# Kernel tuning notes

Measured on AMD Instinct MI355X. Metric: run time of the kernel, lower is better.

The kernel has to match this reference:

```python
import jax, jax.numpy as jnp
import numpy as np

N, E = 100_000, 1_600_000
NDIM_IN, EDIM, F, H, C = 64, 32, 32, 3, 10  # F=ndim_out per head, H=num_heads


def _edge_softmax(scores, dst, n):
    # softmax over incoming edges grouped by destination node (DGL edge_softmax)
    m = jax.ops.segment_max(scores, dst, num_segments=n)          # [N,H]
    ex = jnp.exp(scores - m[dst])                                  # [E,H]
    s = jax.ops.segment_sum(ex, dst, num_segments=n)               # [N,H]
    return ex / s[dst]


def _egat_conv(nf, ef, src, dst, W, We, al, ar, ae, b, n):
    # DGL EdgeGATConv: edge features modulate attention logits only
    h, f = al.shape
    ft = (nf @ W).reshape(-1, h, f)      # [N,H,F]
    fe = (ef @ We).reshape(-1, h, f)     # [E,H,F]
    el = (ft * al).sum(-1)               # [N,H]
    er = (ft * ar).sum(-1)               # [N,H]
    ee = (fe * ae).sum(-1)               # [E,H]
    e = jax.nn.leaky_relu(el[src] + er[dst] + ee, 0.2)             # [E,H]
    a = _edge_softmax(e, dst, n)                                   # [E,H]
    rst = jax.ops.segment_sum(ft[src] * a[:, :, None], dst, num_segments=n)
    return rst + b.reshape(1, h, f)


def setup_inputs() -> dict:
    key = jax.random.key(0)
    ks = jax.random.split(key, 16)
    s = lambda k, shp, fan: (jax.random.normal(k, shp, jnp.float32) / np.sqrt(fan).astype(np.float32))
    d = {}
    d["nfeats"] = jax.random.normal(ks[0], (N, 1, NDIM_IN), jnp.float32)
    d["efeats"] = jax.random.normal(ks[1], (E, 1, EDIM), jnp.float32)
    d["src"] = jax.random.randint(ks[2], (E,), 0, N, jnp.int32)
    d["dst"] = jax.random.randint(ks[3], (E,), 0, N, jnp.int32)
    # conv1 params
    d["W1"] = s(ks[4], (NDIM_IN, H * F), NDIM_IN)
    d["We1"] = s(ks[5], (EDIM, H * F), EDIM)
    d["al1"] = s(ks[6], (H, F), F)
    d["ar1"] = s(ks[7], (H, F), F)
    d["ae1"] = s(ks[8], (H, F), F)
    d["b1"] = jnp.zeros((H * F,), jnp.float32)
    # conv2 params (input dim = H*F after head concat)
    d["W2"] = s(ks[9], (H * F, H * F), H * F)
    d["We2"] = s(ks[10], (EDIM, H * F), EDIM)
    d["al2"] = s(ks[11], (H, F), F)
    d["ar2"] = s(ks[12], (H, F), F)
    d["ae2"] = s(ks[13], (H, F), F)
    d["b2"] = jnp.zeros((H * F,), jnp.float32)
    # edge score head: Linear(2*H*F, C)
    d["Wp"] = s(ks[14], (2 * H * F, C), 2 * H * F)
    d["bp"] = jnp.zeros((C,), jnp.float32)
    return d


def reference(nfeats, efeats, src, dst,
              W1, We1, al1, ar1, ae1, b1,
              W2, We2, al2, ar2, ae2, b2,
              Wp, bp):
    n = nfeats.shape[0]
    nf = jnp.squeeze(nfeats, 1)
    ef = jnp.squeeze(efeats, 1)
    h = _egat_conv(nf, ef, src, dst, W1, We1, al1, ar1, ae1, b1, n)
    h = jax.nn.relu(h.reshape(n, -1))                      # [N, H*F]
    h = _egat_conv(h, ef, src, dst, W2, We2, al2, ar2, ae2, b2, n).reshape(n, -1)
    # MLPPredictor: per-edge cat(h_src, h_dst) -> Linear
    score = jnp.concatenate([h[src], h[dst]], axis=1) @ Wp + bp   # [E, C]
    return score
```

## Files before the change

### kernel.cpp

```cpp
#include <hip/hip_runtime.h>
#include <hip/hip_bf16.h>
#include <stdint.h>

typedef __hip_bfloat16 bf16;

__device__ __forceinline__ float b2f(bf16 x) { return __bfloat162float(x); }
__device__ __forceinline__ float bits2f(uint32_t u) {
    union { uint32_t i; float f; } c; c.i = u; return c.f;
}

__global__ void detect_mode_kernel(const uint16_t* __restrict__ nf, int* __restrict__ flag) {
    if (threadIdx.x != 0 || blockIdx.x != 0) return;
    int sane = 0;
    for (int i = 0; i < 256; ++i) {
        uint32_t u = nf[2 * i];
        float a = fabsf(bits2f(u << 16));
        if (a == 0.f || (a > 1e-5f && a < 100.f)) ++sane;
    }
    flag[0] = (sane >= 128) ? 0 : 1;
}

struct ParamTable {
    const void* src[14];
    int off[15];
};

__global__ void convert_params_kernel(ParamTable T, const int* __restrict__ mode,
                                      float* __restrict__ out) {
    int i = blockIdx.x * blockDim.x + threadIdx.x;
    if (i >= T.off[14]) return;
    int k = 0;
    while (k < 13 && i >= T.off[k + 1]) ++k;
    int j = i - T.off[k];
    out[i] = (*mode == 0) ? b2f(((const bf16*)T.src[k])[j]) : ((const float*)T.src[k])[j];
}

__global__ void fold_wae_kernel(const float* __restrict__ We, const float* __restrict__ ae,
                                float* __restrict__ wae) {
    int t = threadIdx.x;
    if (t >= 96) return;
    int d = t / 3, h = t - d * 3;
    float acc = 0.f;
    for (int f = 0; f < 32; ++f) acc += We[d * 96 + h * 32 + f] * ae[h * 32 + f];
    wae[t] = acc;
}

__global__ void hist_kernel(const int* __restrict__ dst, int* __restrict__ cnt, int E) {
    int e = blockIdx.x * blockDim.x + threadIdx.x;
    if (e < E) atomicAdd(&cnt[dst[e]], 1);
}

__global__ void block_sum_kernel(const int* __restrict__ deg, int* __restrict__ bsums, int N) {
    __shared__ int sd[256];
    int t = threadIdx.x;
    int i = blockIdx.x * 256 + t;
    sd[t] = (i < N) ? deg[i] : 0;
    __syncthreads();
    for (int o = 128; o > 0; o >>= 1) {
        if (t < o) sd[t] += sd[t + o];
        __syncthreads();
    }
    if (t == 0) bsums[blockIdx.x] = sd[0];
}

__global__ void scan_bsums_kernel(int* __restrict__ bsums, int nb) {
    __shared__ int a[512], b[512];
    int t = threadIdx.x;
    int v = (t < nb) ? bsums[t] : 0;
    a[t] = v;
    __syncthreads();
    int* in = a;
    int* out = b;
    for (int o = 1; o < 512; o <<= 1) {
        out[t] = in[t] + ((t >= o) ? in[t - o] : 0);
        __syncthreads();
        int* tmp = in; in = out; out = tmp;
    }
    if (t < nb) bsums[t] = in[t] - v;
}

__global__ void scan_expand_kernel(const int* __restrict__ deg, const int* __restrict__ boffs,
                                   int* __restrict__ row_start, int N) {
    __shared__ int a[256], b[256];
    int t = threadIdx.x;
    int i = blockIdx.x * 256 + t;
    int v = (i < N) ? deg[i] : 0;
    a[t] = v;
    __syncthreads();
    int* in = a;
    int* out = b;
    for (int o = 1; o < 256; o <<= 1) {
        out[t] = in[t] + ((t >= o) ? in[t - o] : 0);
        __syncthreads();
        int* tmp = in; in = out; out = tmp;
    }
    if (i < N) row_start[i] = boffs[blockIdx.x] + in[t] - v;
}

__global__ void set_val_kernel(int* __restrict__ p, int v) { p[0] = v; }

__global__ void scatter_kernel(const int* __restrict__ src, const int* __restrict__ dst,
                               const int* __restrict__ row_start, int* __restrict__ cur,
                               int* __restrict__ csr_edges, int* __restrict__ csr_src,
                               int* __restrict__ csr_dst, int E) {
    int e = blockIdx.x * blockDim.x + threadIdx.x;
    if (e >= E) return;
    int d = dst[e];
    int p = atomicAdd(&cur[d], 1);
    int pos = row_start[d] + p;
    csr_edges[pos] = e;
    csr_src[pos] = src[e];
    csr_dst[pos] = d;
}

__global__ void ft_elr_kernel(const void* __restrict__ X, int kind, const int* __restrict__ mode,
                              int din, const float* __restrict__ W,
                              const float* __restrict__ al, const float* __restrict__ ar,
                              float* __restrict__ ft, float* __restrict__ elr, int N) {
    __shared__ float xs[8 * 96];
    __shared__ float fs[8 * 96];
    int base = blockIdx.x * 8;
    int t = threadIdx.x;
    int m = *mode;
    for (int i = t; i < 8 * din; i += 256) {
        int ln = i / din, d = i - ln * din;
        int node = base + ln;
        float v = 0.f;
        if (node < N) {
            size_t idx = (size_t)node * din + d;
            if (kind == 1)   v = ((const float*)X)[idx];
            else if (m == 0) v = b2f(((const bf16*)X)[idx]);
            else             v = ((const float*)X)[idx];
        }
        xs[ln * 96 + d] = v;
    }
    __syncthreads();
    for (int i = t; i < 768; i += 256) {
        int ln = i / 96, c = i - ln * 96;
        int node = base + ln;
        float acc = 0.f;
        const float* xr = xs + ln * 96;
        for (int d = 0; d < din; ++d) acc += xr[d] * W[d * 96 + c];
        fs[ln * 96 + c] = acc;
        if (node < N) ft[(size_t)node * 96 + c] = acc;
    }
    __syncthreads();
    if (t < 48) {
        int ln = t / 6, q = t - ln * 6;
        int h = q >> 1, isr = q & 1;
        int node = base + ln;
        if (node < N) {
            const float* av = isr ? ar : al;
            const float* fr = fs + ln * 96 + h * 32;
            float acc = 0.f;
            for (int f = 0; f < 32; ++f) acc += fr[f] * av[h * 32 + f];
            elr[node * 6 + isr * 3 + h] = acc;
        }
    }
}

__global__ void edge_pass_csr_kernel(const void* __restrict__ ef, const int* __restrict__ mode,
                                     const float* __restrict__ wae,
                                     const int* __restrict__ csr_edges,
                                     const int* __restrict__ csr_src,
                                     const int* __restrict__ csr_dst,
                                     const float* __restrict__ elr,
                                     float* __restrict__ ex, int E) {
    __shared__ float wsh[96];
    int t = threadIdx.x;
    if (t < 96) wsh[t] = wae[t];
    __syncthreads();
    int i = blockIdx.x * blockDim.x + t;
    if (i >= E) return;
    int m = *mode;
    int eid = csr_edges[i];
    int si = csr_src[i], di = csr_dst[i];

    float x[32];
    if (m == 0) {
        const uint4* p = (const uint4*)((const uint16_t*)ef + (size_t)eid * 32);
#pragma unroll
        for (int q = 0; q < 4; ++q) {
            uint4 u = p[q];
            x[q * 8 + 0] = bits2f(u.x << 16); x[q * 8 + 1] = bits2f(u.x & 0xffff0000u);
            x[q * 8 + 2] = bits2f(u.y << 16); x[q * 8 + 3] = bits2f(u.y & 0xffff0000u);
            x[q * 8 + 4] = bits2f(u.z << 16); x[q * 8 + 5] = bits2f(u.z & 0xffff0000u);
            x[q * 8 + 6] = bits2f(u.w << 16); x[q * 8 + 7] = bits2f(u.w & 0xffff0000u);
        }
    } else {
        const float4* p = (const float4*)((const float*)ef + (size_t)eid * 32);
#pragma unroll
        for (int q = 0; q < 8; ++q) {
            float4 u = p[q];
            x[q * 4 + 0] = u.x; x[q * 4 + 1] = u.y; x[q * 4 + 2] = u.z; x[q * 4 + 3] = u.w;
        }
    }
    float ee0 = 0.f, ee1 = 0.f, ee2 = 0.f;
#pragma unroll
    for (int d = 0; d < 32; ++d) {
        float xv = x[d];
        ee0 += xv * wsh[d * 3 + 0];
        ee1 += xv * wsh[d * 3 + 1];
        ee2 += xv * wsh[d * 3 + 2];
    }
    float l0 = elr[si * 6 + 0] + elr[di * 6 + 3] + ee0;
    float l1 = elr[si * 6 + 1] + elr[di * 6 + 4] + ee1;
    float l2 = elr[si * 6 + 2] + elr[di * 6 + 5] + ee2;
    l0 = (l0 > 0.f) ? l0 : 0.2f * l0;
    l1 = (l1 > 0.f) ? l1 : 0.2f * l1;
    l2 = (l2 > 0.f) ? l2 : 0.2f * l2;
    ex[(size_t)i * 3 + 0] = __expf(l0);
    ex[(size_t)i * 3 + 1] = __expf(l1);
    ex[(size_t)i * 3 + 2] = __expf(l2);
}

__global__ void aggregate_csr_kernel(const float* __restrict__ ft, const float* __restrict__ ex,
                                     const int* __restrict__ row_start,
                                     const int* __restrict__ csr_src,
                                     const float* __restrict__ bias, int do_relu,
                                     float* __restrict__ R, int N) {
    int t = threadIdx.x;
    int node = blockIdx.x * 8 + (t >> 5);
    int lane = t & 31;
    if (node >= N) return;
    int beg = row_start[node], end = row_start[node + 1];
    float a0 = 0.f, a1 = 0.f, a2 = 0.f, s0 = 0.f, s1 = 0.f, s2 = 0.f;
    int i = beg;
    for (; i + 4 <= end; i += 4) {
        int sv0 = csr_src[i], sv1 = csr_src[i + 1], sv2 = csr_src[i + 2], sv3 = csr_src[i + 3];
        const float* f0 = ft + (size_t)sv0 * 96;
        const float* f1 = ft + (size_t)sv1 * 96;
        const float* f2 = ft + (size_t)sv2 * 96;
        const float* f3 = ft + (size_t)sv3 * 96;
        float v00 = f0[lane], v01 = f0[lane + 32], v02 = f0[lane + 64];
        float v10 = f1[lane], v11 = f1[lane + 32], v12 = f1[lane + 64];
        float v20 = f2[lane], v21 = f2[lane + 32], v22 = f2[lane + 64];
        float v30 = f3[lane], v31 = f3[lane + 32], v32 = f3[lane + 64];
        float e00 = ex[(size_t)i * 3 + 0], e01 = ex[(size_t)i * 3 + 1], e02 = ex[(size_t)i * 3 + 2];
        float e10 = ex[(size_t)i * 3 + 3], e11 = ex[(size_t)i * 3 + 4], e12 = ex[(size_t)i * 3 + 5];
        float e20 = ex[(size_t)i * 3 + 6], e21 = ex[(size_t)i * 3 + 7], e22 = ex[(size_t)i * 3 + 8];
        float e30 = ex[(size_t)i * 3 + 9], e31 = ex[(size_t)i * 3 + 10], e32 = ex[(size_t)i * 3 + 11];
        a0 += v00 * e00 + v10 * e10 + v20 * e20 + v30 * e30;
        a1 += v01 * e01 + v11 * e11 + v21 * e21 + v31 * e31;
        a2 += v02 * e02 + v12 * e12 + v22 * e22 + v32 * e32;
        s0 += e00 + e10 + e20 + e30;
        s1 += e01 + e11 + e21 + e31;
        s2 += e02 + e12 + e22 + e32;
    }
    for (; i < end; ++i) {
        int sv = csr_src[i];
        const float* fr = ft + (size_t)sv * 96;
        float e0 = ex[(size_t)i * 3 + 0];
        float e1 = ex[(size_t)i * 3 + 1];
        float e2 = ex[(size_t)i * 3 + 2];
        a0 += fr[lane] * e0;
        a1 += fr[lane + 32] * e1;
        a2 += fr[lane + 64] * e2;
        s0 += e0; s1 += e1; s2 += e2;
    }
    float r0, r1, r2;
    if (end > beg) { r0 = a0 / s0; r1 = a1 / s1; r2 = a2 / s2; }
    else           { r0 = r1 = r2 = 0.f; }
    r0 += bias[lane]; r1 += bias[lane + 32]; r2 += bias[lane + 64];
    if (do_relu) { r0 = fmaxf(r0, 0.f); r1 = fmaxf(r1, 0.f); r2 = fmaxf(r2, 0.f); }
    float* out = R + (size_t)node * 96;
    out[lane] = r0; out[lane + 32] = r1; out[lane + 64] = r2;
}

__global__ void uv_kernel(const float* __restrict__ h, const float* __restrict__ Wp,
                          const float* __restrict__ bp, float* __restrict__ uv, int N) {
    __shared__ float hs[8 * 96];
    int base = blockIdx.x * 8;
    int t = threadIdx.x;
    for (int i = t; i < 768; i += 256) {
        int ln = i / 96, c = i - ln * 96;
        int node = base + ln;
        hs[i] = (node < N) ? h[(size_t)node * 96 + c] : 0.f;
    }
    __syncthreads();
    if (t < 160) {
        int ln = t / 20, q = t - ln * 20;
        int half = q / 10, c = q - half * 10;
        int node = base + ln;
        if (node < N) {
            float acc = half ? 0.f : bp[c];
            const float* hr = hs + ln * 96;
            const float* wcol = Wp + half * 960 + c;
            for (int j = 0; j < 96; ++j) acc += hr[j] * wcol[j * 10];
            uv[node * 20 + q] = acc;
        }
    }
}

__global__ void score_kernel(const float* __restrict__ uv, const int* __restrict__ src,
                             const int* __restrict__ dst, const int* __restrict__ mode,
                             void* __restrict__ out, int E) {
    int e = blockIdx.x * blockDim.x + threadIdx.x;
    if (e >= E) return;
    int si = src[e], di = dst[e];
    const float* u = uv + (size_t)si * 20;
    const float* v = uv + (size_t)di * 20 + 10;
    float r[10];
#pragma unroll
    for (int c = 0; c < 10; ++c) r[c] = u[c] + v[c];
    if (*mode == 0) {
        bf16 o[10];
#pragma unroll
        for (int c = 0; c < 10; ++c) o[c] = __float2bfloat16(r[c]);
        uint32_t* po = (uint32_t*)((bf16*)out + (size_t)e * 10);
        const uint32_t* ps = (const uint32_t*)o;
#pragma unroll
        for (int q = 0; q < 5; ++q) po[q] = ps[q];
    } else {
        float2* po = (float2*)((float*)out + (size_t)e * 10);
#pragma unroll
        for (int q = 0; q < 5; ++q) po[q] = make_float2(r[2 * q], r[2 * q + 1]);
    }
}

extern "C" void kernel_launch(void* const* d_in, const int* in_sizes, int n_in,
                              void* d_out, int out_size, void* d_ws, size_t ws_size,
                              hipStream_t stream) {
    const void* nfeats = d_in[0];
    const void* efeats = d_in[1];
    const int* src = (const int*)d_in[2];
    const int* dst = (const int*)d_in[3];

    const int N = in_sizes[0] / 64;
    const int E = in_sizes[2];

    char* w = (char*)d_ws;
    auto alloc = [&](size_t bytes) {
        void* p = (void*)w;
        w += (bytes + 255) & ~(size_t)255;
        return p;
    };
    int*   flag      = (int*)alloc(256);
    float* pbuf      = (float*)alloc((size_t)24202 * 4);
    float* wae       = (float*)alloc(96 * 4);
    float* R         = (float*)alloc((size_t)N * 96 * 4);
    float* F         = (float*)alloc((size_t)N * 96 * 4);
    float* ex        = (float*)alloc((size_t)E * 3 * 4);
    float* elr       = (float*)alloc((size_t)N * 6 * 4);
    int*   row_start = (int*)alloc((size_t)(N + 1) * 4);
    int*   cnt       = (int*)alloc((size_t)N * 4);
    int*   bsums     = (int*)alloc(512 * 4);
    int*   csr_edges = (int*)alloc((size_t)E * 4);
    int*   csr_src   = (int*)alloc((size_t)E * 4);
    int*   csr_dst   = (int*)alloc((size_t)E * 4);
    float* uv        = ex;

    const int ns[14] = {64*96, 32*96, 96, 96, 96, 96, 96*96, 32*96, 96, 96, 96, 96, 192*10, 10};
    ParamTable T;
    int off = 0;
    for (int k = 0; k < 14; ++k) { T.src[k] = d_in[4 + k]; T.off[k] = off; off += ns[k]; }
    T.off[14] = off;
    float* W1f  = pbuf + T.off[0];
    float* We1f = pbuf + T.off[1];
    float* al1f = pbuf + T.off[2];
    float* ar1f = pbuf + T.off[3];
    float* ae1f = pbuf + T.off[4];
    float* b1f  = pbuf + T.off[5];
    float* W2f  = pbuf + T.off[6];
    float* We2f = pbuf + T.off[7];
    float* al2f = pbuf + T.off[8];
    float* ar2f = pbuf + T.off[9];
    float* ae2f = pbuf + T.off[10];
    float* b2f_ = pbuf + T.off[11];
    float* Wpf  = pbuf + T.off[12];
    float* bpf  = pbuf + T.off[13];

    dim3 b256(256);
    int eblocks    = (E + 255) / 256;
    int nodeBlocks = (N + 7) / 8;
    int nb         = (N + 255) / 256;

    hipLaunchKernelGGL(detect_mode_kernel, dim3(1), dim3(64), 0, stream,
                       (const uint16_t*)nfeats, flag);
    hipLaunchKernelGGL(convert_params_kernel, dim3((off + 255) / 256), b256, 0, stream,
                       T, flag, pbuf);

    hipMemsetAsync(cnt, 0, (size_t)N * 4, stream);
    hipLaunchKernelGGL(hist_kernel, dim3(eblocks), b256, 0, stream, dst, cnt, E);
    hipLaunchKernelGGL(block_sum_kernel, dim3(nb), b256, 0, stream, cnt, bsums, N);
    hipLaunchKernelGGL(scan_bsums_kernel, dim3(1), dim3(512), 0, stream, bsums, nb);
    hipLaunchKernelGGL(scan_expand_kernel, dim3(nb), b256, 0, stream, cnt, bsums, row_start, N);
    hipLaunchKernelGGL(set_val_kernel, dim3(1), dim3(1), 0, stream, row_start + N, E);
    hipMemsetAsync(cnt, 0, (size_t)N * 4, stream);
    hipLaunchKernelGGL(scatter_kernel, dim3(eblocks), b256, 0, stream,
                       src, dst, row_start, cnt, csr_edges, csr_src, csr_dst, E);

    hipLaunchKernelGGL(fold_wae_kernel, dim3(1), dim3(128), 0, stream, We1f, ae1f, wae);
    hipLaunchKernelGGL(ft_elr_kernel, dim3(nodeBlocks), b256, 0, stream,
                       nfeats, 0, flag, 64, W1f, al1f, ar1f, F, elr, N);
    hipLaunchKernelGGL(edge_pass_csr_kernel, dim3(eblocks), b256, 0, stream,
                       efeats, flag, wae, csr_edges, csr_src, csr_dst, elr, ex, E);
    hipLaunchKernelGGL(aggregate_csr_kernel, dim3(nodeBlocks), b256, 0, stream,
                       F, ex, row_start, csr_src, b1f, 1, R, N);

    hipLaunchKernelGGL(fold_wae_kernel, dim3(1), dim3(128), 0, stream, We2f, ae2f, wae);
    hipLaunchKernelGGL(ft_elr_kernel, dim3(nodeBlocks), b256, 0, stream,
                       (const void*)R, 1, flag, 96, W2f, al2f, ar2f, F, elr, N);
    hipLaunchKernelGGL(edge_pass_csr_kernel, dim3(eblocks), b256, 0, stream,
                       efeats, flag, wae, csr_edges, csr_src, csr_dst, elr, ex, E);
    hipLaunchKernelGGL(aggregate_csr_kernel, dim3(nodeBlocks), b256, 0, stream,
                       F, ex, row_start, csr_src, b2f_, 0, R, N);

    hipLaunchKernelGGL(uv_kernel, dim3(nodeBlocks), b256, 0, stream, R, Wpf, bpf, uv, N);
    hipLaunchKernelGGL(score_kernel, dim3(eblocks), b256, 0, stream,
                       uv, src, dst, flag, d_out, E);
}
```

Baseline: 1.195 ms.

## Fuse CSR scatter with edge logits and fold layer-2 edge pass into aggregation

The separate scatter and per-layer edge-pass kernels are replaced by one kernel that reads edge features in original order. It computes both layers' edge attention terms plus the layer-1 exp scores, then scatters them into a packed 32-byte per-edge record in CSR order. Layer-1 aggregation reads the packed records directly. Layer 2 computes logits and exp inside the aggregation kernel from the stored edge term and elr, removing the second edge pass and the gathered edge-feature reads. The cost is a larger per-edge record, scattered 32-byte writes, and extra elr gathers inside aggregation.

```diff
diff --git a/kernel.cpp b/kernel.cpp
--- a/kernel.cpp
+++ b/kernel.cpp
@@ -98,20 +98,6 @@
 }
 
 __global__ void set_val_kernel(int* __restrict__ p, int v) { p[0] = v; }
-
-__global__ void scatter_kernel(const int* __restrict__ src, const int* __restrict__ dst,
-                               const int* __restrict__ row_start, int* __restrict__ cur,
-                               int* __restrict__ csr_edges, int* __restrict__ csr_src,
-                               int* __restrict__ csr_dst, int E) {
-    int e = blockIdx.x * blockDim.x + threadIdx.x;
-    if (e >= E) return;
-    int d = dst[e];
-    int p = atomicAdd(&cur[d], 1);
-    int pos = row_start[d] + p;
-    csr_edges[pos] = e;
-    csr_src[pos] = src[e];
-    csr_dst[pos] = d;
-}
 
 __global__ void ft_elr_kernel(const void* __restrict__ X, int kind, const int* __restrict__ mode,
                               int din, const float* __restrict__ W,
@@ -159,26 +145,24 @@
     }
 }
 
-__global__ void edge_pass_csr_kernel(const void* __restrict__ ef, const int* __restrict__ mode,
-                                     const float* __restrict__ wae,
-                                     const int* __restrict__ csr_edges,
-                                     const int* __restrict__ csr_src,
-                                     const int* __restrict__ csr_dst,
-                                     const float* __restrict__ elr,
-                                     float* __restrict__ ex, int E) {
-    __shared__ float wsh[96];
-    int t = threadIdx.x;
-    if (t < 96) wsh[t] = wae[t];
-    __syncthreads();
-    int i = blockIdx.x * blockDim.x + t;
-    if (i >= E) return;
+__global__ void scatter_edge_kernel(const void* __restrict__ ef, const int* __restrict__ mode,
+                                    const float* __restrict__ wae1, const float* __restrict__ wae2,
+                                    const int* __restrict__ src, const int* __restrict__ dst,
+                                    const float* __restrict__ elr,
+                                    const int* __restrict__ row_start, int* __restrict__ cur,
+                                    float4* __restrict__ S, int E) {
+    __shared__ float w1[96];
+    __shared__ float w2[96];
+    int t = threadIdx.x;
+    if (t < 96) { w1[t] = wae1[t]; w2[t] = wae2[t]; }
+    __syncthreads();
+    int e = blockIdx.x * blockDim.x + t;
+    if (e >= E) return;
     int m = *mode;
-    int eid = csr_edges[i];
-    int si = csr_src[i], di = csr_dst[i];
 
     float x[32];
     if (m == 0) {
-        const uint4* p = (const uint4*)((const uint16_t*)ef + (size_t)eid * 32);
+        const uint4* p = (const uint4*)((const uint16_t*)ef + (size_t)e * 32);
 #pragma unroll
         for (int q = 0; q < 4; ++q) {
             uint4 u = p[q];
@@ -188,37 +172,47 @@
             x[q * 8 + 6] = bits2f(u.w << 16); x[q * 8 + 7] = bits2f(u.w & 0xffff0000u);
         }
     } else {
-        const float4* p = (const float4*)((const float*)ef + (size_t)eid * 32);
+        const float4* p = (const float4*)((const float*)ef + (size_t)e * 32);
 #pragma unroll
         for (int q = 0; q < 8; ++q) {
             float4 u = p[q];
             x[q * 4 + 0] = u.x; x[q * 4 + 1] = u.y; x[q * 4 + 2] = u.z; x[q * 4 + 3] = u.w;
         }
     }
-    float ee0 = 0.f, ee1 = 0.f, ee2 = 0.f;
+    float a0 = 0.f, a1 = 0.f, a2 = 0.f;
+    float c0 = 0.f, c1 = 0.f, c2 = 0.f;
 #pragma unroll
     for (int d = 0; d < 32; ++d) {
         float xv = x[d];
-        ee0 += xv * wsh[d * 3 + 0];
-        ee1 += xv * wsh[d * 3 + 1];
-        ee2 += xv * wsh[d * 3 + 2];
-    }
-    float l0 = elr[si * 6 + 0] + elr[di * 6 + 3] + ee0;
-    float l1 = elr[si * 6 + 1] + elr[di * 6 + 4] + ee1;
-    float l2 = elr[si * 6 + 2] + elr[di * 6 + 5] + ee2;
+        a0 += xv * w1[d * 3 + 0];
+        a1 += xv * w1[d * 3 + 1];
+        a2 += xv * w1[d * 3 + 2];
+        c0 += xv * w2[d * 3 + 0];
+        c1 += xv * w2[d * 3 + 1];
+        c2 += xv * w2[d * 3 + 2];
+    }
+    int si = src[e], di = dst[e];
+    float2 el01 = *(const float2*)(elr + si * 6);
+    float  el2  = elr[si * 6 + 2];
+    float2 er01 = *(const float2*)(elr + di * 6 + 3);
+    float er0 = elr[di * 6 + 3], er1 = elr[di * 6 + 4], er2 = elr[di * 6 + 5];
+    (void)er01;
+    float l0 = el01.x + er0 + a0;
+    float l1 = el01.y + er1 + a1;
+    float l2 = el2    + er2 + a2;
     l0 = (l0 > 0.f) ? l0 : 0.2f * l0;
     l1 = (l1 > 0.f) ? l1 : 0.2f * l1;
     l2 = (l2 > 0.f) ? l2 : 0.2f * l2;
-    ex[(size_t)i * 3 + 0] = __expf(l0);
-    ex[(size_t)i * 3 + 1] = __expf(l1);
-    ex[(size_t)i * 3 + 2] = __expf(l2);
-}
-
-__global__ void aggregate_csr_kernel(const float* __restrict__ ft, const float* __restrict__ ex,
-                                     const int* __restrict__ row_start,
-                                     const int* __restrict__ csr_src,
-                                     const float* __restrict__ bias, int do_relu,
-                                     float* __restrict__ R, int N) {
+    int p = atomicAdd(&cur[di], 1);
+    int pos = row_start[di] + p;
+    S[2 * pos]     = make_float4(__int_as_float(si), __expf(l0), __expf(l1), __expf(l2));
+    S[2 * pos + 1] = make_float4(c0, c1, c2, 0.f);
+}
+
+__global__ void aggregate_direct_kernel(const float* __restrict__ ft, const float4* __restrict__ S,
+                                        const int* __restrict__ row_start,
+                                        const float* __restrict__ bias, int do_relu,
+                                        float* __restrict__ R, int N) {
     int t = threadIdx.x;
     int node = blockIdx.x * 8 + (t >> 5);
     int lane = t & 31;
@@ -227,42 +221,99 @@
     float a0 = 0.f, a1 = 0.f, a2 = 0.f, s0 = 0.f, s1 = 0.f, s2 = 0.f;
     int i = beg;
     for (; i + 4 <= end; i += 4) {
-        int sv0 = csr_src[i], sv1 = csr_src[i + 1], sv2 = csr_src[i + 2], sv3 = csr_src[i + 3];
-        const float* f0 = ft + (size_t)sv0 * 96;
-        const float* f1 = ft + (size_t)sv1 * 96;
-        const float* f2 = ft + (size_t)sv2 * 96;
-        const float* f3 = ft + (size_t)sv3 * 96;
-        float v00 = f0[lane], v01 = f0[lane + 32], v02 = f0[lane + 64];
-        float v10 = f1[lane], v11 = f1[lane + 32], v12 = f1[lane + 64];
-        float v20 = f2[lane], v21 = f2[lane + 32], v22 = f2[lane + 64];
-        float v30 = f3[lane], v31 = f3[lane + 32], v32 = f3[lane + 64];
-        float e00 = ex[(size_t)i * 3 + 0], e01 = ex[(size_t)i * 3 + 1], e02 = ex[(size_t)i * 3 + 2];
-        float e10 = ex[(size_t)i * 3 + 3], e11 = ex[(size_t)i * 3 + 4], e12 = ex[(size_t)i * 3 + 5];
-        float e20 = ex[(size_t)i * 3 + 6], e21 = ex[(size_t)i * 3 + 7], e22 = ex[(size_t)i * 3 + 8];
-        float e30 = ex[(size_t)i * 3 + 9], e31 = ex[(size_t)i * 3 + 10], e32 = ex[(size_t)i * 3 + 11];
-        a0 += v00 * e00 + v10 * e10 + v20 * e20 + v30 * e30;
-        a1 += v01 * e01 + v11 * e11 + v21 * e21 + v31 * e31;
-        a2 += v02 * e02 + v12 * e12 + v22 * e22 + v32 * e32;
-        s0 += e00 + e10 + e20 + e30;
-        s1 += e01 + e11 + e21 + e31;
-        s2 += e02 + e12 + e22 + e32;
+        float4 q0 = S[2 * (i + 0)];
+        float4 q1 = S[2 * (i + 1)];
+        float4 q2 = S[2 * (i + 2)];
+        float4 q3 = S[2 * (i + 3)];
+        int v0 = __float_as_int(q0.x), v1 = __float_as_int(q1.x);
+        int v2 = __float_as_int(q2.x), v3 = __float_as_int(q3.x);
+        const float* f0 = ft + (size_t)v0 * 96;
+        const float* f1 = ft + (size_t)v1 * 96;
+        const float* f2 = ft + (size_t)v2 * 96;
+        const float* f3 = ft + (size_t)v3 * 96;
+        a0 += f0[lane] * q0.y + f1[lane] * q1.y + f2[lane] * q2.y + f3[lane] * q3.y;
+        a1 += f0[lane + 32] * q0.z + f1[lane + 32] * q1.z + f2[lane + 32] * q2.z + f3[lane + 32] * q3.z;
+        a2 += f0[lane + 64] * q0.w + f1[lane + 64] * q1.w + f2[lane + 64] * q2.w + f3[lane + 64] * q3.w;
+        s0 += q0.y + q1.y + q2.y + q3.y;
+        s1 += q0.z + q1.z + q2.z + q3.z;
+        s2 += q0.w + q1.w + q2.w + q3.w;
     }
     for (; i < end; ++i) {
-        int sv = csr_src[i];
+        float4 q = S[2 * i];
+        int sv = __float_as_int(q.x);
         const float* fr = ft + (size_t)sv * 96;
-        float e0 = ex[(size_t)i * 3 + 0];
-        float e1 = ex[(size_t)i * 3 + 1];
-        float e2 = ex[(size_t)i * 3 + 2];
-        a0 += fr[lane] * e0;
-        a1 += fr[lane + 32] * e1;
-        a2 += fr[lane + 64] * e2;
-        s0 += e0; s1 += e1; s2 += e2;
+        a0 += fr[lane] * q.y;
+        a1 += fr[lane + 32] * q.z;
+        a2 += fr[lane + 64] * q.w;
+        s0 += q.y; s1 += q.z; s2 += q.w;
     }
     float r0, r1, r2;
     if (end > beg) { r0 = a0 / s0; r1 = a1 / s1; r2 = a2 / s2; }
     else           { r0 = r1 = r2 = 0.f; }
     r0 += bias[lane]; r1 += bias[lane + 32]; r2 += bias[lane + 64];
     if (do_relu) { r0 = fmaxf(r0, 0.f); r1 = fmaxf(r1, 0.f); r2 = fmaxf(r2, 0.f); }
+    float* out = R + (size_t)node * 96;
+    out[lane] = r0; out[lane + 32] = r1; out[lane + 64] = r2;
+}
+
+__global__ void aggregate_fused_kernel(const float* __restrict__ ft, const float4* __restrict__ S,
+                                       const int* __restrict__ row_start,
+                                       const float* __restrict__ elr,
+                                       const float* __restrict__ bias,
+                                       float* __restrict__ R, int N) {
+    int t = threadIdx.x;
+    int node = blockIdx.x * 8 + (t >> 5);
+    int lane = t & 31;
+    if (node >= N) return;
+    int beg = row_start[node], end = row_start[node + 1];
+    float er0 = elr[node * 6 + 3], er1 = elr[node * 6 + 4], er2 = elr[node * 6 + 5];
+    float a0 = 0.f, a1 = 0.f, a2 = 0.f, s0 = 0.f, s1 = 0.f, s2 = 0.f;
+    int i = beg;
+    for (; i + 4 <= end; i += 4) {
+#pragma unroll
+        for (int u = 0; u < 4; ++u) {
+            float4 qa = S[2 * (i + u)];
+            float4 qb = S[2 * (i + u) + 1];
+            int sv = __float_as_int(qa.x);
+            float2 el01 = *(const float2*)(elr + sv * 6);
+            float  el2  = elr[sv * 6 + 2];
+            float l0 = el01.x + er0 + qb.x;
+            float l1 = el01.y + er1 + qb.y;
+            float l2 = el2    + er2 + qb.z;
+            l0 = (l0 > 0.f) ? l0 : 0.2f * l0;
+            l1 = (l1 > 0.f) ? l1 : 0.2f * l1;
+            l2 = (l2 > 0.f) ? l2 : 0.2f * l2;
+            float e0 = __expf(l0), e1 = __expf(l1), e2 = __expf(l2);
+            const float* fr = ft + (size_t)sv * 96;
+            a0 += fr[lane] * e0;
+            a1 += fr[lane + 32] * e1;
+            a2 += fr[lane + 64] * e2;
+            s0 += e0; s1 += e1; s2 += e2;
+        }
+    }
+    for (; i < end; ++i) {
+        float4 qa = S[2 * i];
+        float4 qb = S[2 * i + 1];
+        int sv = __float_as_int(qa.x);
+        float2 el01 = *(const float2*)(elr + sv * 6);
+        float  el2  = elr[sv * 6 + 2];
+        float l0 = el01.x + er0 + qb.x;
+        float l1 = el01.y + er1 + qb.y;
+        float l2 = el2    + er2 + qb.z;
+        l0 = (l0 > 0.f) ? l0 : 0.2f * l0;
+        l1 = (l1 > 0.f) ? l1 : 0.2f * l1;
+        l2 = (l2 > 0.f) ? l2 : 0.2f * l2;
+        float e0 = __expf(l0), e1 = __expf(l1), e2 = __expf(l2);
+        const float* fr = ft + (size_t)sv * 96;
+        a0 += fr[lane] * e0;
+        a1 += fr[lane + 32] * e1;
+        a2 += fr[lane + 64] * e2;
+        s0 += e0; s1 += e1; s2 += e2;
+    }
+    float r0, r1, r2;
+    if (end > beg) { r0 = a0 / s0; r1 = a1 / s1; r2 = a2 / s2; }
+    else           { r0 = r1 = r2 = 0.f; }
+    r0 += bias[lane]; r1 += bias[lane + 32]; r2 += bias[lane + 64];
     float* out = R + (size_t)node * 96;
     out[lane] = r0; out[lane + 32] = r1; out[lane + 64] = r2;
 }
@@ -335,20 +386,18 @@
         w += (bytes + 255) & ~(size_t)255;
         return p;
     };
-    int*   flag      = (int*)alloc(256);
-    float* pbuf      = (float*)alloc((size_t)24202 * 4);
-    float* wae       = (float*)alloc(96 * 4);
-    float* R         = (float*)alloc((size_t)N * 96 * 4);
-    float* F         = (float*)alloc((size_t)N * 96 * 4);
-    float* ex        = (float*)alloc((size_t)E * 3 * 4);
-    float* elr       = (float*)alloc((size_t)N * 6 * 4);
-    int*   row_start = (int*)alloc((size_t)(N + 1) * 4);
-    int*   cnt       = (int*)alloc((size_t)N * 4);
-    int*   bsums     = (int*)alloc(512 * 4);
-    int*   csr_edges = (int*)alloc((size_t)E * 4);
-    int*   csr_src   = (int*)alloc((size_t)E * 4);
-    int*   csr_dst   = (int*)alloc((size_t)E * 4);
-    float* uv        = ex;
+    int*    flag      = (int*)alloc(256);
+    float*  pbuf      = (float*)alloc((size_t)24202 * 4);
+    float*  wae1      = (float*)alloc(96 * 4);
+    float*  wae2      = (float*)alloc(96 * 4);
+    float*  R         = (float*)alloc((size_t)N * 96 * 4);
+    float*  F         = (float*)alloc((size_t)N * 96 * 4);
+    float4* S         = (float4*)alloc((size_t)E * 32);
+    float*  elr       = (float*)alloc((size_t)N * 6 * 4);
+    int*    row_start = (int*)alloc((size_t)(N + 1) * 4);
+    int*    cnt       = (int*)alloc((size_t)N * 4);
+    int*    bsums     = (int*)alloc(512 * 4);
+    float*  uv        = (float*)S;
 
     const int ns[14] = {64*96, 32*96, 96, 96, 96, 96, 96*96, 32*96, 96, 96, 96, 96, 192*10, 10};
     ParamTable T;
@@ -379,6 +428,8 @@
                        (const uint16_t*)nfeats, flag);
     hipLaunchKernelGGL(convert_params_kernel, dim3((off + 255) / 256), b256, 0, stream,
                        T, flag, pbuf);
+    hipLaunchKernelGGL(fold_wae_kernel, dim3(1), dim3(128), 0, stream, We1f, ae1f, wae1);
+    hipLaunchKernelGGL(fold_wae_kernel, dim3(1), dim3(128), 0, stream, We2f, ae2f, wae2);
 
     hipMemsetAsync(cnt, 0, (size_t)N * 4, stream);
     hipLaunchKernelGGL(hist_kernel, dim3(eblocks), b256, 0, stream, dst, cnt, E);
@@ -386,25 +437,21 @@
     hipLaunchKernelGGL(scan_bsums_kernel, dim3(1), dim3(512), 0, stream, bsums, nb);
     hipLaunchKernelGGL(scan_expand_kernel, dim3(nb), b256, 0, stream, cnt, bsums, row_start, N);
     hipLaunchKernelGGL(set_val_kernel, dim3(1), dim3(1), 0, stream, row_start + N, E);
-    hipMemsetAsync(cnt, 0, (size_t)N * 4, stream);
-    hipLaunchKernelGGL(scatter_kernel, dim3(eblocks), b256, 0, stream,
-                       src, dst, row_start, cnt, csr_edges, csr_src, csr_dst, E);
-
-    hipLaunchKernelGGL(fold_wae_kernel, dim3(1), dim3(128), 0, stream, We1f, ae1f, wae);
+
     hipLaunchKernelGGL(ft_elr_kernel, dim3(nodeBlocks), b256, 0, stream,
                        nfeats, 0, flag, 64, W1f, al1f, ar1f, F, elr, N);
-    hipLaunchKernelGGL(edge_pass_csr_kernel, dim3(eblocks), b256, 0, stream,
-                       efeats, flag, wae, csr_edges, csr_src, csr_dst, elr, ex, E);
-    hipLaunchKernelGGL(aggregate_csr_kernel, dim3(nodeBlocks), b256, 0, stream,
-                       F, ex, row_start, csr_src, b1f, 1, R, N);
-
-    hipLaunchKernelGGL(fold_wae_kernel, dim3(1), dim3(128), 0, stream, We2f, ae2f, wae);
+
+    hipMemsetAsync(cnt, 0, (size_t)N * 4, stream);
+    hipLaunchKernelGGL(scatter_edge_kernel, dim3(eblocks), b256, 0, stream,
+                       efeats, flag, wae1, wae2, src, dst, elr, row_start, cnt, S, E);
+
+    hipLaunchKernelGGL(aggregate_direct_kernel, dim3(nodeBlocks), b256, 0, stream,
+                       F, S, row_start, b1f, 1, R, N);
+
     hipLaunchKernelGGL(ft_elr_kernel, dim3(nodeBlocks), b256, 0, stream,
                        (const void*)R, 1, flag, 96, W2f, al2f, ar2f, F, elr, N);
-    hipLaunchKernelGGL(edge_pass_csr_kernel, dim3(eblocks), b256, 0, stream,
-                       efeats, flag, wae, csr_edges, csr_src, csr_dst, elr, ex, E);
-    hipLaunchKernelGGL(aggregate_csr_kernel, dim3(nodeBlocks), b256, 0, stream,
-                       F, ex, row_start, csr_src, b2f_, 0, R, N);
+    hipLaunchKernelGGL(aggregate_fused_kernel, dim3(nodeBlocks), b256, 0, stream,
+                       F, S, row_start, elr, b2f_, R, N);
 
     hipLaunchKernelGGL(uv_kernel, dim3(nodeBlocks), b256, 0, stream, R, Wpf, bpf, uv, N);
     hipLaunchKernelGGL(score_kernel, dim3(eblocks), b256, 0, stream,
```

Measured after the change: 1.099 ms. 8.0% less time.
